# Kernel optimization log

Measured on AMD Instinct MI355X. Metric: run time of the kernel, lower is better.

The kernel has to match this reference:

```python
import jax, jax.numpy as jnp
import numpy as np

EPS = 1e-12  # torch F.normalize default eps


def _l2norm(x):
    n = jnp.sqrt(jnp.sum(x * x, axis=-1, keepdims=True))
    return x / jnp.maximum(n, EPS)


def setup_inputs() -> dict:
    key = jax.random.key(0)
    ks = jax.random.split(key, 8)
    B, T, V = 4, 2048, 512
    C, H, NB = 512, 4, 64
    return {
        "x": jax.random.normal(ks[0], (B, T, V), dtype=jnp.float32),
        "basis": jax.random.normal(ks[1], (V, 2 * NB), dtype=jnp.float32),
        "shared_q_w": jax.random.normal(ks[2], (V, C), dtype=jnp.float32) * 0.02,
        "shared_k_w": jax.random.normal(ks[3], (V, C), dtype=jnp.float32) * 0.02,
        "v_coeffs": jax.random.normal(ks[4], (C, 2 * NB), dtype=jnp.float32) * 0.02,
        "o_coeffs": jax.random.normal(ks[5], (C, 2 * NB), dtype=jnp.float32) * 0.02,
        "decay_logits": jnp.linspace(1.0, 5.0, H, dtype=jnp.float32),
        "out_scale": jnp.float32(0.1),
    }


def reference(x, basis, shared_q_w, shared_k_w, v_coeffs, o_coeffs, decay_logits, out_scale):
    B, T, V = x.shape
    H = decay_logits.shape[0]
    C = shared_q_w.shape[1]
    D = C // H

    v_w = basis @ v_coeffs.T  # [V, C]
    o_w = basis @ o_coeffs.T  # [V, C]

    q = _l2norm(x @ shared_q_w)  # [B, T, C]
    k = _l2norm(x @ shared_k_w)
    v = x @ v_w

    # [B, H, T, D]
    q = q.reshape(B, T, H, D).transpose(0, 2, 1, 3)
    k = k.reshape(B, T, H, D).transpose(0, 2, 1, 3)
    v = v.reshape(B, T, H, D).transpose(0, 2, 1, 3)

    scores = jnp.einsum("bhqd,bhkd->bhqk", q, k)  # [B, H, T, T]

    decay = jax.nn.sigmoid(decay_logits)  # [H]
    pos = jnp.arange(T)
    diff = pos[None, :] - pos[:, None]  # diff[i, j] = j - i
    mask = (diff > 0).astype(scores.dtype)  # [T, T]
    expo = jnp.clip(diff.astype(jnp.float32) - 1.0, 0.0, None)  # [T, T]
    decay_w = (decay[:, None, None] ** expo[None]) * mask[None]  # [H, T, T]

    scores = scores * decay_w[None].astype(scores.dtype)
    retrieved = jnp.einsum("bhqk,bhkd->bhqd", scores, v)  # [B, H, T, D]
    retrieved = retrieved.transpose(0, 2, 1, 3).reshape(B, T, C)
    return retrieved @ o_w.T * out_scale  # [B, T, V]
```

## Files before the change

kernel.cpp:

```cpp
#include <hip/hip_runtime.h>
#include <hip/hip_bf16.h>

#define BB 4
#define TT 2048
#define VV 512
#define CC 512
#define HH 4
#define DD 128
#define NB2 128
#define NROWS (BB*TT)
#define QC 64
#define NCH (TT/QC)
#define SST 66
#define EPS 1e-12f

typedef __attribute__((ext_vector_type(8))) short bf16x8;
typedef __attribute__((ext_vector_type(4))) float f32x4;
typedef unsigned short u16;

__device__ __forceinline__ void gl_lds16(const void* g, void* l) {
    __builtin_amdgcn_global_load_lds(
        (const __attribute__((address_space(1))) unsigned int*)g,
        (__attribute__((address_space(3))) unsigned int*)l, 16, 0, 0);
}
__device__ __forceinline__ u16 f2bu(float x) {
    __hip_bfloat16 h = __float2bfloat16(x);
    return *reinterpret_cast<u16*>(&h);
}
__device__ __forceinline__ float bu2f(u16 u) {
    __hip_bfloat16 h = *reinterpret_cast<__hip_bfloat16*>(&u);
    return __bfloat162float(h);
}

#define PREP_CVT   4096
#define PREP_TR    512
#define PREP_CB    64
#define PREP_Z     16
__global__ __launch_bounds__(256) void prep_all(
    const float* __restrict__ x, const float* __restrict__ qw,
    const float* __restrict__ kw, const float* __restrict__ basis,
    const float* __restrict__ v_coeffs, const float* __restrict__ o_coeffs,
    const float* __restrict__ out_scale,
    u16* __restrict__ xb, u16* __restrict__ wq, u16* __restrict__ wk,
    u16* __restrict__ bab, u16* __restrict__ vcb, u16* __restrict__ ocb,
    float* __restrict__ norms)
{
    __shared__ float tile[32][33];
    const int bi = blockIdx.x, t = threadIdx.x;
    if (bi < PREP_CVT) {
        int i = bi * 256 + t;
        float4 v = ((const float4*)x)[i];
        u16 h[4] = {f2bu(v.x), f2bu(v.y), f2bu(v.z), f2bu(v.w)};
        ((uint2*)xb)[i] = *(uint2*)h;
    } else if (bi < PREP_CVT + PREP_TR) {
        int id = bi - PREP_CVT;
        const int z = id >> 8; id &= 255;
        const float* in = z ? kw : qw;
        u16* outT = z ? wk : wq;
        const int bx = (id & 15) * 32, by = (id >> 4) * 32;
        const int tx = t & 31, ty = t >> 5;
        #pragma unroll
        for (int r = 0; r < 32; r += 8)
            tile[ty + r][tx] = in[(size_t)(by + ty + r) * CC + bx + tx];
        __syncthreads();
        #pragma unroll
        for (int r = 0; r < 32; r += 8)
            outT[(size_t)(bx + ty + r) * VV + by + tx] = f2bu(tile[tx][ty + r]);
    } else if (bi < PREP_CVT + PREP_TR + 3 * PREP_CB) {
        int id = bi - PREP_CVT - PREP_TR;
        const int which = id / PREP_CB;
        int i = (id - which * PREP_CB) * 256 + t;
        const float* src = which == 0 ? basis : (which == 1 ? v_coeffs : o_coeffs);
        u16* dst = which == 0 ? bab : (which == 1 ? vcb : ocb);
        const float sc = which == 2 ? out_scale[0] : 1.f;
        float4 v = ((const float4*)src)[i];
        u16 h[4] = {f2bu(v.x * sc), f2bu(v.y * sc), f2bu(v.z * sc), f2bu(v.w * sc)};
        ((uint2*)dst)[i] = *(uint2*)h;
    } else {
        int idx = (bi - PREP_CVT - PREP_TR - 3 * PREP_CB) * 256 + t;
        ((float4*)norms)[idx] = make_float4(0.f, 0.f, 0.f, 0.f);
    }
}

__device__ __forceinline__ void gemm_body(
    const u16* __restrict__ A, const u16* __restrict__ Bt,
    u16* __restrict__ Cp, int N, int K, int m0, int n0,
    u16* __restrict__ As, u16* __restrict__ Bs)
{
    const int t = threadIdx.x;
    const int wave = t >> 6, lane = t & 63;
    const int qq = lane >> 4, l16 = lane & 15;
    const int wm = (wave >> 1) * 64, wn = (wave & 1) * 64;

    const int s0 = wave * 128 + lane, s1 = s0 + 64;
    const int r0_ = s0 >> 2, c0_ = ((s0 & 3) - (r0_ >> 1)) & 3;
    const int r1_ = s1 >> 2, c1_ = ((s1 & 3) - (r1_ >> 1)) & 3;
    const u16* ga0 = A  + (size_t)(m0 + r0_) * K + c0_ * 8;
    const u16* ga1 = A  + (size_t)(m0 + r1_) * K + c1_ * 8;
    const u16* gb0 = Bt + (size_t)(n0 + r0_) * K + c0_ * 8;
    const u16* gb1 = Bt + (size_t)(n0 + r1_) * K + c1_ * 8;
    const int lo0 = (wave * 128) * 8, lo1 = (wave * 128 + 64) * 8;

    gl_lds16(ga0, As + lo0);
    gl_lds16(ga1, As + lo1);
    gl_lds16(gb0, Bs + lo0);
    gl_lds16(gb1, Bs + lo1);

    f32x4 acc[4][4];
    #pragma unroll
    for (int i = 0; i < 4; ++i)
        #pragma unroll
        for (int j = 0; j < 4; ++j) acc[i][j] = (f32x4){0.f, 0.f, 0.f, 0.f};

    int ib = 0;
    for (int k0 = 0; k0 < K; k0 += 32, ib ^= 1) {
        __syncthreads();
        if (k0 + 32 < K) {
            const int off = (ib ^ 1) * 4096;
            gl_lds16(ga0 + k0 + 32, As + off + lo0);
            gl_lds16(ga1 + k0 + 32, As + off + lo1);
            gl_lds16(gb0 + k0 + 32, Bs + off + lo0);
            gl_lds16(gb1 + k0 + 32, Bs + off + lo1);
        }
        const u16* Ac = As + ib * 4096;
        const u16* Bc = Bs + ib * 4096;
        bf16x8 af[4], bfr[4];
        #pragma unroll
        for (int mt = 0; mt < 4; ++mt) {
            const int r = wm + mt * 16 + l16;
            af[mt] = *(const bf16x8*)&Ac[(r * 4 + ((qq + (r >> 1)) & 3)) * 8];
        }
        #pragma unroll
        for (int nt = 0; nt < 4; ++nt) {
            const int r = wn + nt * 16 + l16;
            bfr[nt] = *(const bf16x8*)&Bc[(r * 4 + ((qq + (r >> 1)) & 3)) * 8];
        }
        #pragma unroll
        for (int mt = 0; mt < 4; ++mt)
            #pragma unroll
            for (int nt = 0; nt < 4; ++nt)
                acc[mt][nt] = __builtin_amdgcn_mfma_f32_16x16x32_bf16(
                    af[mt], bfr[nt], acc[mt][nt], 0, 0, 0);
    }
    #pragma unroll
    for (int mt = 0; mt < 4; ++mt)
        #pragma unroll
        for (int r = 0; r < 4; ++r) {
            int grow = m0 + wm + mt * 16 + qq * 4 + r;
            #pragma unroll
            for (int nt = 0; nt < 4; ++nt)
                Cp[(size_t)grow * N + n0 + wn + nt * 16 + l16] = f2bu(acc[mt][nt][r]);
        }
}

__global__ __launch_bounds__(256) void gemm_w(
    const u16* __restrict__ bab, const u16* __restrict__ vcb,
    const u16* __restrict__ ocb, u16* __restrict__ v_wT, u16* __restrict__ o_ws)
{
    __shared__ __align__(16) u16 As[8192];
    __shared__ __align__(16) u16 Bs[8192];
    const int sec = blockIdx.x >> 2;
    const u16* A  = sec ? bab : vcb;
    const u16* Bt = sec ? ocb : bab;
    u16* C = sec ? o_ws : v_wT;
    gemm_body(A, Bt, C, 512, NB2, blockIdx.y * 128, (blockIdx.x & 3) * 128, As, Bs);
}

__global__ __launch_bounds__(256, 1) void gemm_qkv_fused(
    const u16* __restrict__ xb, const u16* __restrict__ wcat,
    u16* __restrict__ qo, u16* __restrict__ ko, u16* __restrict__ vo,
    float* __restrict__ norms)
{
    __shared__ __align__(16) u16 As[2 * 4096];
    __shared__ __align__(16) u16 Bs[3 * 2 * 4096];
    const int t = threadIdx.x;
    const int wave = t >> 6, lane = t & 63;
    const int qq = lane >> 4, l16 = lane & 15;
    const int m0 = blockIdx.y * 128, n0 = blockIdx.x * 128;
    const int wm = (wave >> 1) * 64, wn = (wave & 1) * 64;
    const int K = VV;

    const int s0 = wave * 128 + lane, s1 = s0 + 64;
    const int r0_ = s0 >> 2, c0_ = ((s0 & 3) - (r0_ >> 1)) & 3;
    const int r1_ = s1 >> 2, c1_ = ((s1 & 3) - (r1_ >> 1)) & 3;
    const u16* ga0 = xb + (size_t)(m0 + r0_) * K + c0_ * 8;
    const u16* ga1 = xb + (size_t)(m0 + r1_) * K + c1_ * 8;
    const u16* gb0[3];
    const u16* gb1[3];
    #pragma unroll
    for (int sec = 0; sec < 3; ++sec) {
        gb0[sec] = wcat + (size_t)sec * VV * CC + (size_t)(n0 + r0_) * K + c0_ * 8;
        gb1[sec] = wcat + (size_t)sec * VV * CC + (size_t)(n0 + r1_) * K + c1_ * 8;
    }
    const int lo0 = (wave * 128) * 8, lo1 = lo0 + 512;

    gl_lds16(ga0, As + lo0);
    gl_lds16(ga1, As + lo1);
    #pragma unroll
    for (int sec = 0; sec < 3; ++sec) {
        gl_lds16(gb0[sec], Bs + sec * 8192 + lo0);
        gl_lds16(gb1[sec], Bs + sec * 8192 + lo1);
    }

    f32x4 acc[3][4][4];
    #pragma unroll
    for (int s = 0; s < 3; ++s)
        #pragma unroll
        for (int i = 0; i < 4; ++i)
            #pragma unroll
            for (int j = 0; j < 4; ++j) acc[s][i][j] = (f32x4){0.f, 0.f, 0.f, 0.f};

    int ib = 0;
    for (int k0 = 0; k0 < K; k0 += 32, ib ^= 1) {
        __syncthreads();
        if (k0 + 32 < K) {
            const int off = (ib ^ 1) * 4096;
            gl_lds16(ga0 + k0 + 32, As + off + lo0);
            gl_lds16(ga1 + k0 + 32, As + off + lo1);
            #pragma unroll
            for (int sec = 0; sec < 3; ++sec) {
                gl_lds16(gb0[sec] + k0 + 32, Bs + sec * 8192 + off + lo0);
                gl_lds16(gb1[sec] + k0 + 32, Bs + sec * 8192 + off + lo1);
            }
        }
        const u16* Ac = As + ib * 4096;
        bf16x8 af[4];
        #pragma unroll
        for (int mt = 0; mt < 4; ++mt) {
            const int r = wm + mt * 16 + l16;
            af[mt] = *(const bf16x8*)&Ac[(r * 4 + ((qq + (r >> 1)) & 3)) * 8];
        }
        #pragma unroll
        for (int sec = 0; sec < 3; ++sec) {
            const u16* Bc = Bs + sec * 8192 + ib * 4096;
            bf16x8 bfr[4];
            #pragma unroll
            for (int nt = 0; nt < 4; ++nt) {
                const int r = wn + nt * 16 + l16;
                bfr[nt] = *(const bf16x8*)&Bc[(r * 4 + ((qq + (r >> 1)) & 3)) * 8];
            }
            #pragma unroll
            for (int mt = 0; mt < 4; ++mt)
                #pragma unroll
                for (int nt = 0; nt < 4; ++nt)
                    acc[sec][mt][nt] = __builtin_amdgcn_mfma_f32_16x16x32_bf16(
                        af[mt], bfr[nt], acc[sec][mt][nt], 0, 0, 0);
        }
    }
    #pragma unroll
    for (int sec = 0; sec < 3; ++sec) {
        u16* outp = sec == 0 ? qo : (sec == 1 ? ko : vo);
        #pragma unroll
        for (int mt = 0; mt < 4; ++mt)
            #pragma unroll
            for (int r = 0; r < 4; ++r) {
                int grow = m0 + wm + mt * 16 + qq * 4 + r;
                #pragma unroll
                for (int nt = 0; nt < 4; ++nt)
                    outp[(size_t)grow * CC + n0 + wn + nt * 16 + l16] =
                        f2bu(acc[sec][mt][nt][r]);
            }
        if (sec < 2) {
            float* np = sec == 0 ? norms : norms + NROWS;
            #pragma unroll
            for (int mt = 0; mt < 4; ++mt)
                #pragma unroll
                for (int r = 0; r < 4; ++r) {
                    float s = 0.f;
                    #pragma unroll
                    for (int nt = 0; nt < 4; ++nt) {
                        float v = acc[sec][mt][nt][r];
                        s = fmaf(v, v, s);
                    }
                    s += __shfl_xor(s, 1, 64);
                    s += __shfl_xor(s, 2, 64);
                    s += __shfl_xor(s, 4, 64);
                    s += __shfl_xor(s, 8, 64);
                    if (l16 == 0)
                        atomicAdd(&np[m0 + wm + mt * 16 + qq * 4 + r], s);
                }
        }
    }
}

__global__ __launch_bounds__(256) void gemm_out64(
    const u16* __restrict__ A, const u16* __restrict__ Bt, float* __restrict__ C)
{
    __shared__ __align__(16) u16 As[4096];
    __shared__ __align__(16) u16 Bs[8192];
    const int t = threadIdx.x;
    const int wave = t >> 6, lane = t & 63;
    const int qq = lane >> 4, l16 = lane & 15;
    const int m0 = blockIdx.y * 64, n0 = blockIdx.x * 128;
    const int wm = (wave >> 1) * 32, wn = (wave & 1) * 64;
    const int N = VV, K = CC;

    const int sA = wave * 64 + lane;
    const int rA = sA >> 2, cA = ((sA & 3) - (rA >> 1)) & 3;
    const int sB0 = wave * 128 + lane, sB1 = sB0 + 64;
    const int rB0 = sB0 >> 2, cB0 = ((sB0 & 3) - (rB0 >> 1)) & 3;
    const int rB1 = sB1 >> 2, cB1 = ((sB1 & 3) - (rB1 >> 1)) & 3;
    const u16* ga  = A  + (size_t)(m0 + rA) * K + cA * 8;
    const u16* gb0 = Bt + (size_t)(n0 + rB0) * K + cB0 * 8;
    const u16* gb1 = Bt + (size_t)(n0 + rB1) * K + cB1 * 8;
    const int loA = wave * 512, loB0 = wave * 1024, loB1 = wave * 1024 + 512;

    gl_lds16(ga, As + loA);
    gl_lds16(gb0, Bs + loB0);
    gl_lds16(gb1, Bs + loB1);

    f32x4 acc[2][4];
    #pragma unroll
    for (int i = 0; i < 2; ++i)
        #pragma unroll
        for (int j = 0; j < 4; ++j) acc[i][j] = (f32x4){0.f, 0.f, 0.f, 0.f};

    int ib = 0;
    for (int k0 = 0; k0 < K; k0 += 32, ib ^= 1) {
        __syncthreads();
        if (k0 + 32 < K) {
            gl_lds16(ga + k0 + 32,  As + (ib ^ 1) * 2048 + loA);
            gl_lds16(gb0 + k0 + 32, Bs + (ib ^ 1) * 4096 + loB0);
            gl_lds16(gb1 + k0 + 32, Bs + (ib ^ 1) * 4096 + loB1);
        }
        const u16* Ac = As + ib * 2048;
        const u16* Bc = Bs + ib * 4096;
        bf16x8 af[2], bfr[4];
        #pragma unroll
        for (int mt = 0; mt < 2; ++mt) {
            const int r = wm + mt * 16 + l16;
            af[mt] = *(const bf16x8*)&Ac[(r * 4 + ((qq + (r >> 1)) & 3)) * 8];
        }
        #pragma unroll
        for (int nt = 0; nt < 4; ++nt) {
            const int r = wn + nt * 16 + l16;
            bfr[nt] = *(const bf16x8*)&Bc[(r * 4 + ((qq + (r >> 1)) & 3)) * 8];
        }
        #pragma unroll
        for (int mt = 0; mt < 2; ++mt)
            #pragma unroll
            for (int nt = 0; nt < 4; ++nt)
                acc[mt][nt] = __builtin_amdgcn_mfma_f32_16x16x32_bf16(
                    af[mt], bfr[nt], acc[mt][nt], 0, 0, 0);
    }
    #pragma unroll
    for (int mt = 0; mt < 2; ++mt)
        #pragma unroll
        for (int r = 0; r < 4; ++r) {
            int grow = m0 + wm + mt * 16 + qq * 4 + r;
            #pragma unroll
            for (int nt = 0; nt < 4; ++nt)
                C[(size_t)grow * N + n0 + wn + nt * 16 + l16] = acc[mt][nt][r];
        }
}

__global__ __launch_bounds__(256) void state_local(
    const u16* __restrict__ kb, const u16* __restrict__ vb,
    const float* __restrict__ norms_k, const float* __restrict__ dlog,
    u16* __restrict__ statesb)
{
    __shared__ __align__(16) u16 vT[DD][SST];
    __shared__ __align__(16) u16 kT[DD][SST];
    const int c = blockIdx.x, bh = blockIdx.y;
    const int b = bh >> 2, h = bh & 3;
    const float lam = 1.f / (1.f + __expf(-dlog[h]));
    const float l2lam = log2f(lam);
    const int t = threadIdx.x;
    const int row0 = b * TT + c * QC;
    const size_t gbase = (size_t)row0 * CC + h * DD;

    {
        const int j2 = t & 31, d0 = (t >> 5) * 16;
        const int jj0 = 2 * j2, jj1 = jj0 + 1;
        const float w0 = exp2f((float)jj0 * l2lam);
        const float w1 = exp2f((float)jj1 * l2lam);
        const float rk0 = 1.f / fmaxf(sqrtf(norms_k[row0 + jj0]), EPS);
        const float rk1 = 1.f / fmaxf(sqrtf(norms_k[row0 + jj1]), EPS);
        u16 k0a[16], k1a[16], v0a[16], v1a[16];
        const u16* k0p = kb + gbase + (size_t)jj0 * CC + d0;
        const u16* k1p = kb + gbase + (size_t)jj1 * CC + d0;
        const u16* v0p = vb + gbase + (size_t)jj0 * CC + d0;
        const u16* v1p = vb + gbase + (size_t)jj1 * CC + d0;
        *(uint4*)&k0a[0] = *(const uint4*)k0p; *(uint4*)&k0a[8] = *(const uint4*)(k0p + 8);
        *(uint4*)&k1a[0] = *(const uint4*)k1p; *(uint4*)&k1a[8] = *(const uint4*)(k1p + 8);
        *(uint4*)&v0a[0] = *(const uint4*)v0p; *(uint4*)&v0a[8] = *(const uint4*)(v0p + 8);
        *(uint4*)&v1a[0] = *(const uint4*)v1p; *(uint4*)&v1a[8] = *(const uint4*)(v1p + 8);
        #pragma unroll
        for (int i = 0; i < 16; ++i) {
            unsigned int kw = (unsigned int)f2bu(bu2f(k0a[i]) * rk0)
                            | ((unsigned int)f2bu(bu2f(k1a[i]) * rk1) << 16);
            *(unsigned int*)&kT[d0 + i][jj0] = kw;
            unsigned int vw = (unsigned int)f2bu(bu2f(v0a[i]) * w0)
                            | ((unsigned int)f2bu(bu2f(v1a[i]) * w1) << 16);
            *(unsigned int*)&vT[d0 + i][jj0] = vw;
        }
    }
    __syncthreads();

    const int wave = t >> 6, lane = t & 63;
    const int quad = lane >> 4, l16 = lane & 15;
    f32x4 acc[2][8];
    #pragma unroll
    for (int i = 0; i < 2; ++i)
        #pragma unroll
        for (int j = 0; j < 8; ++j) acc[i][j] = (f32x4){0.f, 0.f, 0.f, 0.f};

    #pragma unroll
    for (int s = 0; s < 2; ++s) {
        bf16x8 af[2];
        #pragma unroll
        for (int mt = 0; mt < 2; ++mt)
            af[mt] = *(const bf16x8*)&vT[wave * 32 + mt * 16 + l16][s * 32 + quad * 8];
        #pragma unroll
        for (int nt = 0; nt < 8; ++nt) {
            bf16x8 bk = *(const bf16x8*)&kT[nt * 16 + l16][s * 32 + quad * 8];
            #pragma unroll
            for (int mt = 0; mt < 2; ++mt)
                acc[mt][nt] = __builtin_amdgcn_mfma_f32_16x16x32_bf16(
                    af[mt], bk, acc[mt][nt], 0, 0, 0);
        }
    }
    u16* so = statesb + ((size_t)(bh * NCH + c) << 14);
    #pragma unroll
    for (int mt = 0; mt < 2; ++mt)
        #pragma unroll
        for (int rr = 0; rr < 4; ++rr) {
            const int d = wave * 32 + mt * 16 + quad * 4 + rr;
            #pragma unroll
            for (int nt = 0; nt < 8; ++nt)
                so[(size_t)d * DD + nt * 16 + l16] = f2bu(acc[mt][nt][rr]);
        }
}

__global__ __launch_bounds__(256) void state_combine(
    const float* __restrict__ dlog, u16* __restrict__ statesb)
{
    const int bh = blockIdx.x >> 3, part = blockIdx.x & 7;
    const int h = bh & 3;
    const float lam = 1.f / (1.f + __expf(-dlog[h]));
    const float lamQ = exp2f((float)QC * log2f(lam));
    const int t = threadIdx.x;
    float run[8] = {};
    uint4* pbase = (uint4*)(statesb + ((size_t)(bh * NCH) << 14)) + part * 256 + t;
    uint4 cur = pbase[(size_t)(NCH - 1) * 2048];
    for (int c = NCH - 1; c >= 0; --c) {
        uint4 nxt = cur;
        if (c) nxt = pbase[(size_t)(c - 1) * 2048];
        u16* hb = (u16*)&cur;
        uint4 outw;
        u16* ho = (u16*)&outw;
        #pragma unroll
        for (int i = 0; i < 8; ++i) {
            float tmp = bu2f(hb[i]);
            ho[i] = f2bu(run[i]);
            run[i] = fmaf(lamQ, run[i], tmp);
        }
        pbase[(size_t)c * 2048] = outw;
        cur = nxt;
    }
}

__global__ __launch_bounds__(256) void attention_fused(
    const u16* __restrict__ qb, const u16* __restrict__ kb,
    const u16* __restrict__ vb, const u16* __restrict__ statesb,
    const float* __restrict__ norms, const float* __restrict__ dlog,
    u16* __restrict__ retb)
{
    __shared__ __align__(16) u16 qks[2 * QC * DD];
    __shared__ __align__(16) u16 vsT[DD][SST];
    __shared__ __align__(16) u16 ss[QC][SST];
    __shared__ float rql[QC], rkl[QC];

    const int c = blockIdx.x, bh = blockIdx.y;
    const int b = bh >> 2, h = bh & 3;
    const float lam = 1.f / (1.f + __expf(-dlog[h]));
    const float l2lam = log2f(lam);
    const int t = threadIdx.x;
    const int row0 = b * TT + c * QC;
    const size_t base = (size_t)row0 * CC + h * DD;

    const int wave = t >> 6, lane = t & 63;
    const int quad = lane >> 4, l16 = lane & 15;
    const int r0 = wave * 16;

    {
        const int lrow = lane >> 4, cch = lane & 15;
        #pragma unroll
        for (int u = 0; u < 4; ++u) {
            const int R = wave * 16 + u * 4;
            const int gr = R + lrow;
            const int cq = (cch - gr) & 15;
            gl_lds16(qb + base + (size_t)gr * CC + cq * 8, &qks[R * DD]);
            gl_lds16(kb + base + (size_t)gr * CC + cq * 8, &qks[(QC + R) * DD]);
        }
    }
    if (t < QC)            rql[t]      = 1.f / fmaxf(sqrtf(norms[row0 + t]), EPS);
    else if (t < 2 * QC)   rkl[t - QC] = 1.f / fmaxf(sqrtf(norms[NROWS + row0 + t - QC]), EPS);
    {
        const int j2 = t & 31, d0 = (t >> 5) * 16;
        const u16* v0 = vb + base + (size_t)(2 * j2) * CC + d0;
        const u16* v1 = v0 + CC;
        uint4 a0 = *(const uint4*)v0;
        uint4 a1 = *(const uint4*)(v0 + 8);
        uint4 b0 = *(const uint4*)v1;
        uint4 b1 = *(const uint4*)(v1 + 8);
        const u16* ap0 = (const u16*)&a0; const u16* ap1 = (const u16*)&a1;
        const u16* bp0 = (const u16*)&b0; const u16* bp1 = (const u16*)&b1;
        #pragma unroll
        for (int i = 0; i < 8; ++i) {
            *(unsigned int*)&vsT[d0 + i][2 * j2] =
                (unsigned int)ap0[i] | ((unsigned int)bp0[i] << 16);
            *(unsigned int*)&vsT[d0 + 8 + i][2 * j2] =
                (unsigned int)ap1[i] | ((unsigned int)bp1[i] << 16);
        }
    }
    __syncthreads();

    bf16x8 aq[4];
    #pragma unroll
    for (int kq = 0; kq < 4; ++kq) {
        const int r = r0 + l16;
        aq[kq] = *(const bf16x8*)&qks[r * DD + ((kq * 4 + quad + r) & 15) * 8];
    }

    f32x4 accs[4];
    #pragma unroll
    for (int nt = 0; nt < 4; ++nt) accs[nt] = (f32x4){0.f, 0.f, 0.f, 0.f};
    #pragma unroll
    for (int nt = 0; nt < 4; ++nt)
        #pragma unroll
        for (int kq = 0; kq < 4; ++kq) {
            const int rk_ = nt * 16 + l16;
            bf16x8 bk = *(const bf16x8*)&qks[(QC + rk_) * DD + ((kq * 4 + quad + rk_) & 15) * 8];
            accs[nt] = __builtin_amdgcn_mfma_f32_16x16x32_bf16(aq[kq], bk, accs[nt], 0, 0, 0);
        }

    #pragma unroll
    for (int nt = 0; nt < 4; ++nt) {
        const int j = nt * 16 + l16;
        const float rkj = rkl[j];
        #pragma unroll
        for (int rr = 0; rr < 4; ++rr) {
            const int i = r0 + quad * 4 + rr;
            const int di = j - i;
            float p = (di > 0) ? accs[nt][rr] * exp2f((float)(di - 1) * l2lam) * rkj : 0.f;
            ss[i][j] = f2bu(p);
        }
    }
    __syncthreads();

    const u16* sb = statesb + ((size_t)(bh * NCH + c) << 14);
    {
        const int drow = lane >> 4, cch = lane & 15;
        #pragma unroll
        for (int u = 0; u < 8; ++u) {
            const int D = wave * 32 + u * 4;
            const int gd = D + drow;
            const int cq = (cch - gd) & 15;
            gl_lds16(sb + (size_t)gd * DD + cq * 8, &qks[D * DD]);
        }
    }
    bf16x8 ap[2];
    #pragma unroll
    for (int kj = 0; kj < 2; ++kj)
        ap[kj] = *(const bf16x8*)&ss[r0 + l16][kj * 32 + quad * 8];
    f32x4 accd[8];
    #pragma unroll
    for (int nt = 0; nt < 8; ++nt) accd[nt] = (f32x4){0.f, 0.f, 0.f, 0.f};
    #pragma unroll
    for (int nt = 0; nt < 8; ++nt)
        #pragma unroll
        for (int kj = 0; kj < 2; ++kj) {
            bf16x8 bv = *(const bf16x8*)&vsT[nt * 16 + l16][kj * 32 + quad * 8];
            accd[nt] = __builtin_amdgcn_mfma_f32_16x16x32_bf16(ap[kj], bv, accd[nt], 0, 0, 0);
        }
    __syncthreads();

    f32x4 accc[8];
    #pragma unroll
    for (int nt = 0; nt < 8; ++nt) accc[nt] = (f32x4){0.f, 0.f, 0.f, 0.f};
    #pragma unroll
    for (int nt = 0; nt < 8; ++nt)
        #pragma unroll
        for (int kq = 0; kq < 4; ++kq) {
            const int d = nt * 16 + l16;
            bf16x8 bs_ = *(const bf16x8*)&qks[d * DD + ((kq * 4 + quad + d) & 15) * 8];
            accc[nt] = __builtin_amdgcn_mfma_f32_16x16x32_bf16(aq[kq], bs_, accc[nt], 0, 0, 0);
        }

    u16* rb = retb + (size_t)row0 * CC + h * DD;
    #pragma unroll
    for (int rr = 0; rr < 4; ++rr) {
        const int ii = r0 + quad * 4 + rr;
        const float wrow = exp2f((float)(QC - 1 - ii) * l2lam);
        const float rq = rql[ii];
        #pragma unroll
        for (int nt = 0; nt < 8; ++nt) {
            float val = (accd[nt][rr] + wrow * accc[nt][rr]) * rq;
            rb[(size_t)ii * CC + nt * 16 + l16] = f2bu(val);
        }
    }
}

extern "C" void kernel_launch(void* const* d_in, const int* in_sizes, int n_in,
                              void* d_out, int out_size, void* d_ws, size_t ws_size,
                              hipStream_t stream) {
    const float* x         = (const float*)d_in[0];
    const float* basis     = (const float*)d_in[1];
    const float* qw        = (const float*)d_in[2];
    const float* kw        = (const float*)d_in[3];
    const float* v_coeffs  = (const float*)d_in[4];
    const float* o_coeffs  = (const float*)d_in[5];
    const float* dlog      = (const float*)d_in[6];
    const float* out_scale = (const float*)d_in[7];
    float* out             = (float*)d_out;

    u16* p = (u16*)d_ws;
    u16* qb      = p;
    u16* kb      = qb + (size_t)NROWS * CC;
    u16* vb      = kb + (size_t)NROWS * CC;
    u16* statesb = vb + (size_t)NROWS * CC;
    u16* xb      = statesb + (size_t)BB * HH * NCH * DD * DD;
    u16* retb    = xb;
    u16* wcat    = xb + (size_t)NROWS * CC;
    u16* o_ws    = wcat + 3 * (size_t)VV * CC;
    float* norms = (float*)(o_ws + (size_t)VV * CC);
    u16* bab     = (u16*)(norms + 2 * NROWS);
    u16* vcb     = bab + (size_t)VV * NB2;
    u16* ocb     = vcb + (size_t)VV * NB2;

    prep_all<<<PREP_CVT + PREP_TR + 3 * PREP_CB + PREP_Z, 256, 0, stream>>>(
        x, qw, kw, basis, v_coeffs, o_coeffs, out_scale,
        xb, wcat, wcat + (size_t)VV * CC, bab, vcb, ocb, norms);
    gemm_w<<<dim3(8, 4), 256, 0, stream>>>(bab, vcb, ocb,
                                           wcat + 2 * (size_t)VV * CC, o_ws);
    gemm_qkv_fused<<<dim3(4, NROWS / 128), 256, 0, stream>>>(xb, wcat, qb, kb, vb,
                                                             norms);
    state_local  <<<dim3(NCH, BB * HH), 256, 0, stream>>>(kb, vb, norms + NROWS,
                                                          dlog, statesb);
    state_combine<<<BB * HH * 8, 256, 0, stream>>>(dlog, statesb);
    attention_fused<<<dim3(NCH, BB * HH), 256, 0, stream>>>(qb, kb, vb, statesb,
                                                            norms, dlog, retb);
    gemm_out64<<<dim3(VV / 128, NROWS / 64), 256, 0, stream>>>(retb, o_ws, out);
}
```

Baseline: 168.0 us.

## Fuse weight GEMM into prep kernel and merge tail stages into one cooperative kernel

```diff
diff --git a/kernel.cpp b/kernel.cpp
--- a/kernel.cpp
+++ b/kernel.cpp
@@ -1,5 +1,8 @@
 #include <hip/hip_runtime.h>
 #include <hip/hip_bf16.h>
+#include <hip/hip_cooperative_groups.h>
+
+namespace cg = cooperative_groups;
 
 #define BB 4
 #define TT 2048
@@ -31,29 +34,36 @@
     __hip_bfloat16 h = *reinterpret_cast<__hip_bfloat16*>(&u);
     return __bfloat162float(h);
 }
-
-#define PREP_CVT   4096
-#define PREP_TR    512
-#define PREP_CB    64
-#define PREP_Z     16
-__global__ __launch_bounds__(256) void prep_all(
+__device__ __forceinline__ uint4 pack8(float4 a, float4 b, float s) {
+    u16 h[8] = {f2bu(a.x * s), f2bu(a.y * s), f2bu(a.z * s), f2bu(a.w * s),
+                f2bu(b.x * s), f2bu(b.y * s), f2bu(b.z * s), f2bu(b.w * s)};
+    return *(uint4*)h;
+}
+
+#define P2_CVT 4096
+#define P2_TR  512
+#define P2_Z   16
+#define P2_WG  32
+__global__ __launch_bounds__(256) void prep_all2(
     const float* __restrict__ x, const float* __restrict__ qw,
     const float* __restrict__ kw, const float* __restrict__ basis,
     const float* __restrict__ v_coeffs, const float* __restrict__ o_coeffs,
     const float* __restrict__ out_scale,
     u16* __restrict__ xb, u16* __restrict__ wq, u16* __restrict__ wk,
-    u16* __restrict__ bab, u16* __restrict__ vcb, u16* __restrict__ ocb,
-    float* __restrict__ norms)
+    u16* __restrict__ v_wT, u16* __restrict__ o_ws, float* __restrict__ norms)
 {
-    __shared__ float tile[32][33];
+    __shared__ __align__(16) union {
+        float tile[32][33];
+        struct { u16 A[4096]; u16 B[4096]; } w;
+    } sm;
     const int bi = blockIdx.x, t = threadIdx.x;
-    if (bi < PREP_CVT) {
+    if (bi < P2_CVT) {
         int i = bi * 256 + t;
         float4 v = ((const float4*)x)[i];
         u16 h[4] = {f2bu(v.x), f2bu(v.y), f2bu(v.z), f2bu(v.w)};
         ((uint2*)xb)[i] = *(uint2*)h;
-    } else if (bi < PREP_CVT + PREP_TR) {
-        int id = bi - PREP_CVT;
+    } else if (bi < P2_CVT + P2_TR) {
+        int id = bi - P2_CVT;
         const int z = id >> 8; id &= 255;
         const float* in = z ? kw : qw;
         u16* outT = z ? wk : wq;
@@ -61,109 +71,74 @@
         const int tx = t & 31, ty = t >> 5;
         #pragma unroll
         for (int r = 0; r < 32; r += 8)
-            tile[ty + r][tx] = in[(size_t)(by + ty + r) * CC + bx + tx];
+            sm.tile[ty + r][tx] = in[(size_t)(by + ty + r) * CC + bx + tx];
         __syncthreads();
         #pragma unroll
         for (int r = 0; r < 32; r += 8)
-            outT[(size_t)(bx + ty + r) * VV + by + tx] = f2bu(tile[tx][ty + r]);
-    } else if (bi < PREP_CVT + PREP_TR + 3 * PREP_CB) {
-        int id = bi - PREP_CVT - PREP_TR;
-        const int which = id / PREP_CB;
-        int i = (id - which * PREP_CB) * 256 + t;
-        const float* src = which == 0 ? basis : (which == 1 ? v_coeffs : o_coeffs);
-        u16* dst = which == 0 ? bab : (which == 1 ? vcb : ocb);
-        const float sc = which == 2 ? out_scale[0] : 1.f;
-        float4 v = ((const float4*)src)[i];
-        u16 h[4] = {f2bu(v.x * sc), f2bu(v.y * sc), f2bu(v.z * sc), f2bu(v.w * sc)};
-        ((uint2*)dst)[i] = *(uint2*)h;
+            outT[(size_t)(bx + ty + r) * VV + by + tx] = f2bu(sm.tile[tx][ty + r]);
+    } else if (bi < P2_CVT + P2_TR + P2_Z) {
+        int idx = (bi - P2_CVT - P2_TR) * 256 + t;
+        ((float4*)norms)[idx] = make_float4(0.f, 0.f, 0.f, 0.f);
     } else {
-        int idx = (bi - PREP_CVT - PREP_TR - 3 * PREP_CB) * 256 + t;
-        ((float4*)norms)[idx] = make_float4(0.f, 0.f, 0.f, 0.f);
-    }
-}
-
-__device__ __forceinline__ void gemm_body(
-    const u16* __restrict__ A, const u16* __restrict__ Bt,
-    u16* __restrict__ Cp, int N, int K, int m0, int n0,
-    u16* __restrict__ As, u16* __restrict__ Bs)
-{
-    const int t = threadIdx.x;
-    const int wave = t >> 6, lane = t & 63;
-    const int qq = lane >> 4, l16 = lane & 15;
-    const int wm = (wave >> 1) * 64, wn = (wave & 1) * 64;
-
-    const int s0 = wave * 128 + lane, s1 = s0 + 64;
-    const int r0_ = s0 >> 2, c0_ = ((s0 & 3) - (r0_ >> 1)) & 3;
-    const int r1_ = s1 >> 2, c1_ = ((s1 & 3) - (r1_ >> 1)) & 3;
-    const u16* ga0 = A  + (size_t)(m0 + r0_) * K + c0_ * 8;
-    const u16* ga1 = A  + (size_t)(m0 + r1_) * K + c1_ * 8;
-    const u16* gb0 = Bt + (size_t)(n0 + r0_) * K + c0_ * 8;
-    const u16* gb1 = Bt + (size_t)(n0 + r1_) * K + c1_ * 8;
-    const int lo0 = (wave * 128) * 8, lo1 = (wave * 128 + 64) * 8;
-
-    gl_lds16(ga0, As + lo0);
-    gl_lds16(ga1, As + lo1);
-    gl_lds16(gb0, Bs + lo0);
-    gl_lds16(gb1, Bs + lo1);
-
-    f32x4 acc[4][4];
-    #pragma unroll
-    for (int i = 0; i < 4; ++i)
-        #pragma unroll
-        for (int j = 0; j < 4; ++j) acc[i][j] = (f32x4){0.f, 0.f, 0.f, 0.f};
-
-    int ib = 0;
-    for (int k0 = 0; k0 < K; k0 += 32, ib ^= 1) {
-        __syncthreads();
-        if (k0 + 32 < K) {
-            const int off = (ib ^ 1) * 4096;
-            gl_lds16(ga0 + k0 + 32, As + off + lo0);
-            gl_lds16(ga1 + k0 + 32, As + off + lo1);
-            gl_lds16(gb0 + k0 + 32, Bs + off + lo0);
-            gl_lds16(gb1 + k0 + 32, Bs + off + lo1);
-        }
-        const u16* Ac = As + ib * 4096;
-        const u16* Bc = Bs + ib * 4096;
-        bf16x8 af[4], bfr[4];
-        #pragma unroll
-        for (int mt = 0; mt < 4; ++mt) {
-            const int r = wm + mt * 16 + l16;
-            af[mt] = *(const bf16x8*)&Ac[(r * 4 + ((qq + (r >> 1)) & 3)) * 8];
-        }
-        #pragma unroll
-        for (int nt = 0; nt < 4; ++nt) {
-            const int r = wn + nt * 16 + l16;
-            bfr[nt] = *(const bf16x8*)&Bc[(r * 4 + ((qq + (r >> 1)) & 3)) * 8];
+        int id = bi - (P2_CVT + P2_TR + P2_Z);
+        const int sec = id >> 4, rem = id & 15;
+        const int m0 = (rem >> 2) * 128, n0 = (rem & 3) * 128;
+        const float* Af = sec ? basis : v_coeffs;
+        const float* Bf = sec ? o_coeffs : basis;
+        u16* Cp = sec ? o_ws : v_wT;
+        const float scB = sec ? out_scale[0] : 1.f;
+        const int wave = t >> 6, lane = t & 63;
+        const int qq = lane >> 4, l16 = lane & 15;
+        const int wm = (wave >> 1) * 64, wn = (wave & 1) * 64;
+        const int s0 = wave * 128 + lane, s1 = s0 + 64;
+        const int r0 = s0 >> 2, c0 = ((s0 & 3) - (r0 >> 1)) & 3;
+        const int r1 = s1 >> 2, c1 = ((s1 & 3) - (r1 >> 1)) & 3;
+        f32x4 acc[4][4];
+        #pragma unroll
+        for (int i = 0; i < 4; ++i)
+            #pragma unroll
+            for (int j = 0; j < 4; ++j) acc[i][j] = (f32x4){0.f, 0.f, 0.f, 0.f};
+        for (int k0 = 0; k0 < NB2; k0 += 32) {
+            __syncthreads();
+            {
+                const float* p0 = Af + (size_t)(m0 + r0) * NB2 + k0 + c0 * 8;
+                const float* p1 = Af + (size_t)(m0 + r1) * NB2 + k0 + c1 * 8;
+                *(uint4*)&sm.w.A[s0 * 8] = pack8(((const float4*)p0)[0], ((const float4*)p0)[1], 1.f);
+                *(uint4*)&sm.w.A[s1 * 8] = pack8(((const float4*)p1)[0], ((const float4*)p1)[1], 1.f);
+                const float* q0 = Bf + (size_t)(n0 + r0) * NB2 + k0 + c0 * 8;
+                const float* q1 = Bf + (size_t)(n0 + r1) * NB2 + k0 + c1 * 8;
+                *(uint4*)&sm.w.B[s0 * 8] = pack8(((const float4*)q0)[0], ((const float4*)q0)[1], scB);
+                *(uint4*)&sm.w.B[s1 * 8] = pack8(((const float4*)q1)[0], ((const float4*)q1)[1], scB);
+            }
+            __syncthreads();
+            bf16x8 af[4], bfr[4];
+            #pragma unroll
+            for (int mt = 0; mt < 4; ++mt) {
+                const int r = wm + mt * 16 + l16;
+                af[mt] = *(const bf16x8*)&sm.w.A[(r * 4 + ((qq + (r >> 1)) & 3)) * 8];
+            }
+            #pragma unroll
+            for (int nt = 0; nt < 4; ++nt) {
+                const int r = wn + nt * 16 + l16;
+                bfr[nt] = *(const bf16x8*)&sm.w.B[(r * 4 + ((qq + (r >> 1)) & 3)) * 8];
+            }
+            #pragma unroll
+            for (int mt = 0; mt < 4; ++mt)
+                #pragma unroll
+                for (int nt = 0; nt < 4; ++nt)
+                    acc[mt][nt] = __builtin_amdgcn_mfma_f32_16x16x32_bf16(
+                        af[mt], bfr[nt], acc[mt][nt], 0, 0, 0);
         }
         #pragma unroll
         for (int mt = 0; mt < 4; ++mt)
             #pragma unroll
-            for (int nt = 0; nt < 4; ++nt)
-                acc[mt][nt] = __builtin_amdgcn_mfma_f32_16x16x32_bf16(
-                    af[mt], bfr[nt], acc[mt][nt], 0, 0, 0);
-    }
-    #pragma unroll
-    for (int mt = 0; mt < 4; ++mt)
-        #pragma unroll
-        for (int r = 0; r < 4; ++r) {
-            int grow = m0 + wm + mt * 16 + qq * 4 + r;
-            #pragma unroll
-            for (int nt = 0; nt < 4; ++nt)
-                Cp[(size_t)grow * N + n0 + wn + nt * 16 + l16] = f2bu(acc[mt][nt][r]);
-        }
-}
-
-__global__ __launch_bounds__(256) void gemm_w(
-    const u16* __restrict__ bab, const u16* __restrict__ vcb,
-    const u16* __restrict__ ocb, u16* __restrict__ v_wT, u16* __restrict__ o_ws)
-{
-    __shared__ __align__(16) u16 As[8192];
-    __shared__ __align__(16) u16 Bs[8192];
-    const int sec = blockIdx.x >> 2;
-    const u16* A  = sec ? bab : vcb;
-    const u16* Bt = sec ? ocb : bab;
-    u16* C = sec ? o_ws : v_wT;
-    gemm_body(A, Bt, C, 512, NB2, blockIdx.y * 128, (blockIdx.x & 3) * 128, As, Bs);
+            for (int rr = 0; rr < 4; ++rr) {
+                int grow = m0 + wm + mt * 16 + qq * 4 + rr;
+                #pragma unroll
+                for (int nt = 0; nt < 4; ++nt)
+                    Cp[(size_t)grow * 512 + n0 + wn + nt * 16 + l16] = f2bu(acc[mt][nt][rr]);
+            }
+    }
 }
 
 __global__ __launch_bounds__(256, 1) void gemm_qkv_fused(
@@ -283,322 +258,305 @@
     }
 }
 
-__global__ __launch_bounds__(256) void gemm_out64(
-    const u16* __restrict__ A, const u16* __restrict__ Bt, float* __restrict__ C)
+__global__ __launch_bounds__(256, 2) void tail_coop(
+    const u16* __restrict__ qb, const u16* __restrict__ kb,
+    const u16* __restrict__ vb, u16* __restrict__ statesb,
+    const float* __restrict__ norms, const float* __restrict__ dlog,
+    u16* __restrict__ retb, const u16* __restrict__ o_ws,
+    float* __restrict__ out)
 {
-    __shared__ __align__(16) u16 As[4096];
-    __shared__ __align__(16) u16 Bs[8192];
+    cg::grid_group gg = cg::this_grid();
+    __shared__ __align__(16) union {
+        struct { u16 vT[DD][SST]; u16 kT[DD][SST]; } pa;
+        struct { u16 qks[2 * QC * DD]; u16 vsT[DD][SST]; u16 ss[QC][SST];
+                 float rql[QC]; float rkl[QC]; } pc;
+        struct { u16 As[4096]; u16 Bs[8192]; } pd;
+    } sm;
+
     const int t = threadIdx.x;
     const int wave = t >> 6, lane = t & 63;
-    const int qq = lane >> 4, l16 = lane & 15;
-    const int m0 = blockIdx.y * 64, n0 = blockIdx.x * 128;
-    const int wm = (wave >> 1) * 32, wn = (wave & 1) * 64;
-    const int N = VV, K = CC;
-
-    const int sA = wave * 64 + lane;
-    const int rA = sA >> 2, cA = ((sA & 3) - (rA >> 1)) & 3;
-    const int sB0 = wave * 128 + lane, sB1 = sB0 + 64;
-    const int rB0 = sB0 >> 2, cB0 = ((sB0 & 3) - (rB0 >> 1)) & 3;
-    const int rB1 = sB1 >> 2, cB1 = ((sB1 & 3) - (rB1 >> 1)) & 3;
-    const u16* ga  = A  + (size_t)(m0 + rA) * K + cA * 8;
-    const u16* gb0 = Bt + (size_t)(n0 + rB0) * K + cB0 * 8;
-    const u16* gb1 = Bt + (size_t)(n0 + rB1) * K + cB1 * 8;
-    const int loA = wave * 512, loB0 = wave * 1024, loB1 = wave * 1024 + 512;
-
-    gl_lds16(ga, As + loA);
-    gl_lds16(gb0, Bs + loB0);
-    gl_lds16(gb1, Bs + loB1);
-
-    f32x4 acc[2][4];
-    #pragma unroll
-    for (int i = 0; i < 2; ++i)
-        #pragma unroll
-        for (int j = 0; j < 4; ++j) acc[i][j] = (f32x4){0.f, 0.f, 0.f, 0.f};
-
-    int ib = 0;
-    for (int k0 = 0; k0 < K; k0 += 32, ib ^= 1) {
-        __syncthreads();
-        if (k0 + 32 < K) {
-            gl_lds16(ga + k0 + 32,  As + (ib ^ 1) * 2048 + loA);
-            gl_lds16(gb0 + k0 + 32, Bs + (ib ^ 1) * 4096 + loB0);
-            gl_lds16(gb1 + k0 + 32, Bs + (ib ^ 1) * 4096 + loB1);
-        }
-        const u16* Ac = As + ib * 2048;
-        const u16* Bc = Bs + ib * 4096;
-        bf16x8 af[2], bfr[4];
-        #pragma unroll
-        for (int mt = 0; mt < 2; ++mt) {
-            const int r = wm + mt * 16 + l16;
-            af[mt] = *(const bf16x8*)&Ac[(r * 4 + ((qq + (r >> 1)) & 3)) * 8];
-        }
-        #pragma unroll
-        for (int nt = 0; nt < 4; ++nt) {
-            const int r = wn + nt * 16 + l16;
-            bfr[nt] = *(const bf16x8*)&Bc[(r * 4 + ((qq + (r >> 1)) & 3)) * 8];
-        }
-        #pragma unroll
-        for (int mt = 0; mt < 2; ++mt)
-            #pragma unroll
-            for (int nt = 0; nt < 4; ++nt)
-                acc[mt][nt] = __builtin_amdgcn_mfma_f32_16x16x32_bf16(
-                    af[mt], bfr[nt], acc[mt][nt], 0, 0, 0);
-    }
-    #pragma unroll
-    for (int mt = 0; mt < 2; ++mt)
-        #pragma unroll
-        for (int r = 0; r < 4; ++r) {
-            int grow = m0 + wm + mt * 16 + qq * 4 + r;
-            #pragma unroll
-            for (int nt = 0; nt < 4; ++nt)
-                C[(size_t)grow * N + n0 + wn + nt * 16 + l16] = acc[mt][nt][r];
-        }
-}
-
-__global__ __launch_bounds__(256) void state_local(
-    const u16* __restrict__ kb, const u16* __restrict__ vb,
-    const float* __restrict__ norms_k, const float* __restrict__ dlog,
-    u16* __restrict__ statesb)
-{
-    __shared__ __align__(16) u16 vT[DD][SST];
-    __shared__ __align__(16) u16 kT[DD][SST];
-    const int c = blockIdx.x, bh = blockIdx.y;
+    const int quad = lane >> 4, l16 = lane & 15;
+    const int cx = blockIdx.x, bh = blockIdx.y;
     const int b = bh >> 2, h = bh & 3;
     const float lam = 1.f / (1.f + __expf(-dlog[h]));
     const float l2lam = log2f(lam);
-    const int t = threadIdx.x;
-    const int row0 = b * TT + c * QC;
-    const size_t gbase = (size_t)row0 * CC + h * DD;
 
     {
-        const int j2 = t & 31, d0 = (t >> 5) * 16;
-        const int jj0 = 2 * j2, jj1 = jj0 + 1;
-        const float w0 = exp2f((float)jj0 * l2lam);
-        const float w1 = exp2f((float)jj1 * l2lam);
-        const float rk0 = 1.f / fmaxf(sqrtf(norms_k[row0 + jj0]), EPS);
-        const float rk1 = 1.f / fmaxf(sqrtf(norms_k[row0 + jj1]), EPS);
-        u16 k0a[16], k1a[16], v0a[16], v1a[16];
-        const u16* k0p = kb + gbase + (size_t)jj0 * CC + d0;
-        const u16* k1p = kb + gbase + (size_t)jj1 * CC + d0;
-        const u16* v0p = vb + gbase + (size_t)jj0 * CC + d0;
-        const u16* v1p = vb + gbase + (size_t)jj1 * CC + d0;
-        *(uint4*)&k0a[0] = *(const uint4*)k0p; *(uint4*)&k0a[8] = *(const uint4*)(k0p + 8);
-        *(uint4*)&k1a[0] = *(const uint4*)k1p; *(uint4*)&k1a[8] = *(const uint4*)(k1p + 8);
-        *(uint4*)&v0a[0] = *(const uint4*)v0p; *(uint4*)&v0a[8] = *(const uint4*)(v0p + 8);
-        *(uint4*)&v1a[0] = *(const uint4*)v1p; *(uint4*)&v1a[8] = *(const uint4*)(v1p + 8);
-        #pragma unroll
-        for (int i = 0; i < 16; ++i) {
-            unsigned int kw = (unsigned int)f2bu(bu2f(k0a[i]) * rk0)
-                            | ((unsigned int)f2bu(bu2f(k1a[i]) * rk1) << 16);
-            *(unsigned int*)&kT[d0 + i][jj0] = kw;
-            unsigned int vw = (unsigned int)f2bu(bu2f(v0a[i]) * w0)
-                            | ((unsigned int)f2bu(bu2f(v1a[i]) * w1) << 16);
-            *(unsigned int*)&vT[d0 + i][jj0] = vw;
-        }
-    }
-    __syncthreads();
-
-    const int wave = t >> 6, lane = t & 63;
-    const int quad = lane >> 4, l16 = lane & 15;
-    f32x4 acc[2][8];
-    #pragma unroll
-    for (int i = 0; i < 2; ++i)
-        #pragma unroll
-        for (int j = 0; j < 8; ++j) acc[i][j] = (f32x4){0.f, 0.f, 0.f, 0.f};
-
-    #pragma unroll
-    for (int s = 0; s < 2; ++s) {
-        bf16x8 af[2];
+        const int row0 = b * TT + cx * QC;
+        const size_t gbase = (size_t)row0 * CC + h * DD;
+        {
+            const int j2 = t & 31, d0 = (t >> 5) * 16;
+            const int jj0 = 2 * j2, jj1 = jj0 + 1;
+            const float w0 = exp2f((float)jj0 * l2lam);
+            const float w1 = exp2f((float)jj1 * l2lam);
+            const float rk0 = 1.f / fmaxf(sqrtf(norms[NROWS + row0 + jj0]), EPS);
+            const float rk1 = 1.f / fmaxf(sqrtf(norms[NROWS + row0 + jj1]), EPS);
+            u16 k0a[16], k1a[16], v0a[16], v1a[16];
+            const u16* k0p = kb + gbase + (size_t)jj0 * CC + d0;
+            const u16* k1p = kb + gbase + (size_t)jj1 * CC + d0;
+            const u16* v0p = vb + gbase + (size_t)jj0 * CC + d0;
+            const u16* v1p = vb + gbase + (size_t)jj1 * CC + d0;
+            *(uint4*)&k0a[0] = *(const uint4*)k0p; *(uint4*)&k0a[8] = *(const uint4*)(k0p + 8);
+            *(uint4*)&k1a[0] = *(const uint4*)k1p; *(uint4*)&k1a[8] = *(const uint4*)(k1p + 8);
+            *(uint4*)&v0a[0] = *(const uint4*)v0p; *(uint4*)&v0a[8] = *(const uint4*)(v0p + 8);
+            *(uint4*)&v1a[0] = *(const uint4*)v1p; *(uint4*)&v1a[8] = *(const uint4*)(v1p + 8);
+            #pragma unroll
+            for (int i = 0; i < 16; ++i) {
+                unsigned int kw = (unsigned int)f2bu(bu2f(k0a[i]) * rk0)
+                                | ((unsigned int)f2bu(bu2f(k1a[i]) * rk1) << 16);
+                *(unsigned int*)&sm.pa.kT[d0 + i][jj0] = kw;
+                unsigned int vw = (unsigned int)f2bu(bu2f(v0a[i]) * w0)
+                                | ((unsigned int)f2bu(bu2f(v1a[i]) * w1) << 16);
+                *(unsigned int*)&sm.pa.vT[d0 + i][jj0] = vw;
+            }
+        }
+        __syncthreads();
+
+        f32x4 acc[2][8];
+        #pragma unroll
+        for (int i = 0; i < 2; ++i)
+            #pragma unroll
+            for (int j = 0; j < 8; ++j) acc[i][j] = (f32x4){0.f, 0.f, 0.f, 0.f};
+
+        #pragma unroll
+        for (int s = 0; s < 2; ++s) {
+            bf16x8 af[2];
+            #pragma unroll
+            for (int mt = 0; mt < 2; ++mt)
+                af[mt] = *(const bf16x8*)&sm.pa.vT[wave * 32 + mt * 16 + l16][s * 32 + quad * 8];
+            #pragma unroll
+            for (int nt = 0; nt < 8; ++nt) {
+                bf16x8 bk = *(const bf16x8*)&sm.pa.kT[nt * 16 + l16][s * 32 + quad * 8];
+                #pragma unroll
+                for (int mt = 0; mt < 2; ++mt)
+                    acc[mt][nt] = __builtin_amdgcn_mfma_f32_16x16x32_bf16(
+                        af[mt], bk, acc[mt][nt], 0, 0, 0);
+            }
+        }
+        u16* so = statesb + ((size_t)(bh * NCH + cx) << 14);
         #pragma unroll
         for (int mt = 0; mt < 2; ++mt)
-            af[mt] = *(const bf16x8*)&vT[wave * 32 + mt * 16 + l16][s * 32 + quad * 8];
-        #pragma unroll
-        for (int nt = 0; nt < 8; ++nt) {
-            bf16x8 bk = *(const bf16x8*)&kT[nt * 16 + l16][s * 32 + quad * 8];
+            #pragma unroll
+            for (int rr = 0; rr < 4; ++rr) {
+                const int d = wave * 32 + mt * 16 + quad * 4 + rr;
+                #pragma unroll
+                for (int nt = 0; nt < 8; ++nt)
+                    so[(size_t)d * DD + nt * 16 + l16] = f2bu(acc[mt][nt][rr]);
+            }
+    }
+    __threadfence();
+    gg.sync();
+
+    {
+        const float lamQ = exp2f((float)QC * l2lam);
+        unsigned int* pb = (unsigned int*)(statesb + ((size_t)(bh * NCH) << 14))
+                           + cx * 256 + t;
+        float run0 = 0.f, run1 = 0.f;
+        unsigned int cur = pb[(size_t)(NCH - 1) * 8192];
+        for (int c2 = NCH - 1; c2 >= 0; --c2) {
+            unsigned int nxt = cur;
+            if (c2) nxt = pb[(size_t)(c2 - 1) * 8192];
+            float t0 = bu2f((u16)(cur & 0xffffu));
+            float t1 = bu2f((u16)(cur >> 16));
+            unsigned int outw = (unsigned int)f2bu(run0)
+                              | ((unsigned int)f2bu(run1) << 16);
+            pb[(size_t)c2 * 8192] = outw;
+            run0 = fmaf(lamQ, run0, t0);
+            run1 = fmaf(lamQ, run1, t1);
+            cur = nxt;
+        }
+    }
+    __threadfence();
+    gg.sync();
+
+    {
+        const int row0 = b * TT + cx * QC;
+        const size_t base = (size_t)row0 * CC + h * DD;
+        const int r0 = wave * 16;
+        {
+            const int lrow = lane >> 4, cch = lane & 15;
+            #pragma unroll
+            for (int u = 0; u < 4; ++u) {
+                const int R = wave * 16 + u * 4;
+                const int gr = R + lrow;
+                const int cq = (cch - gr) & 15;
+                gl_lds16(qb + base + (size_t)gr * CC + cq * 8, &sm.pc.qks[R * DD]);
+                gl_lds16(kb + base + (size_t)gr * CC + cq * 8, &sm.pc.qks[(QC + R) * DD]);
+            }
+        }
+        if (t < QC)            sm.pc.rql[t]      = 1.f / fmaxf(sqrtf(norms[row0 + t]), EPS);
+        else if (t < 2 * QC)   sm.pc.rkl[t - QC] = 1.f / fmaxf(sqrtf(norms[NROWS + row0 + t - QC]), EPS);
+        {
+            const int j2 = t & 31, d0 = (t >> 5) * 16;
+            const u16* v0 = vb + base + (size_t)(2 * j2) * CC + d0;
+            const u16* v1 = v0 + CC;
+            uint4 a0 = *(const uint4*)v0;
+            uint4 a1 = *(const uint4*)(v0 + 8);
+            uint4 b0 = *(const uint4*)v1;
+            uint4 b1 = *(const uint4*)(v1 + 8);
+            const u16* ap0 = (const u16*)&a0; const u16* ap1 = (const u16*)&a1;
+            const u16* bp0 = (const u16*)&b0; const u16* bp1 = (const u16*)&b1;
+            #pragma unroll
+            for (int i = 0; i < 8; ++i) {
+                *(unsigned int*)&sm.pc.vsT[d0 + i][2 * j2] =
+                    (unsigned int)ap0[i] | ((unsigned int)bp0[i] << 16);
+                *(unsigned int*)&sm.pc.vsT[d0 + 8 + i][2 * j2] =
+                    (unsigned int)ap1[i] | ((unsigned int)bp1[i] << 16);
+            }
+        }
+        __syncthreads();
+
+        bf16x8 aq[4];
+        #pragma unroll
+        for (int kq = 0; kq < 4; ++kq) {
+            const int r = r0 + l16;
+            aq[kq] = *(const bf16x8*)&sm.pc.qks[r * DD + ((kq * 4 + quad + r) & 15) * 8];
+        }
+
+        f32x4 accs[4];
+        #pragma unroll
+        for (int nt = 0; nt < 4; ++nt) accs[nt] = (f32x4){0.f, 0.f, 0.f, 0.f};
+        #pragma unroll
+        for (int nt = 0; nt < 4; ++nt)
+            #pragma unroll
+            for (int kq = 0; kq < 4; ++kq) {
+                const int rk_ = nt * 16 + l16;
+                bf16x8 bk = *(const bf16x8*)&sm.pc.qks[(QC + rk_) * DD + ((kq * 4 + quad + rk_) & 15) * 8];
+                accs[nt] = __builtin_amdgcn_mfma_f32_16x16x32_bf16(aq[kq], bk, accs[nt], 0, 0, 0);
+            }
+
+        #pragma unroll
+        for (int nt = 0; nt < 4; ++nt) {
+            const int j = nt * 16 + l16;
+            const float rkj = sm.pc.rkl[j];
+            #pragma unroll
+            for (int rr = 0; rr < 4; ++rr) {
+                const int i = r0 + quad * 4 + rr;
+                const int di = j - i;
+                float p = (di > 0) ? accs[nt][rr] * exp2f((float)(di - 1) * l2lam) * rkj : 0.f;
+                sm.pc.ss[i][j] = f2bu(p);
+            }
+        }
+        __syncthreads();
+
+        const u16* sb = statesb + ((size_t)(bh * NCH + cx) << 14);
+        {
+            const int drow = lane >> 4, cch = lane & 15;
+            #pragma unroll
+            for (int u = 0; u < 8; ++u) {
+                const int D_ = wave * 32 + u * 4;
+                const int gd = D_ + drow;
+                const int cq = (cch - gd) & 15;
+                gl_lds16(sb + (size_t)gd * DD + cq * 8, &sm.pc.qks[D_ * DD]);
+            }
+        }
+        bf16x8 app[2];
+        #pragma unroll
+        for (int kj = 0; kj < 2; ++kj)
+            app[kj] = *(const bf16x8*)&sm.pc.ss[r0 + l16][kj * 32 + quad * 8];
+        f32x4 accd[8];
+        #pragma unroll
+        for (int nt = 0; nt < 8; ++nt) accd[nt] = (f32x4){0.f, 0.f, 0.f, 0.f};
+        #pragma unroll
+        for (int nt = 0; nt < 8; ++nt)
+            #pragma unroll
+            for (int kj = 0; kj < 2; ++kj) {
+                bf16x8 bv = *(const bf16x8*)&sm.pc.vsT[nt * 16 + l16][kj * 32 + quad * 8];
+                accd[nt] = __builtin_amdgcn_mfma_f32_16x16x32_bf16(app[kj], bv, accd[nt], 0, 0, 0);
+            }
+        __syncthreads();
+
+        f32x4 accc[8];
+        #pragma unroll
+        for (int nt = 0; nt < 8; ++nt) accc[nt] = (f32x4){0.f, 0.f, 0.f, 0.f};
+        #pragma unroll
+        for (int nt = 0; nt < 8; ++nt)
+            #pragma unroll
+            for (int kq = 0; kq < 4; ++kq) {
+                const int d = nt * 16 + l16;
+                bf16x8 bs_ = *(const bf16x8*)&sm.pc.qks[d * DD + ((kq * 4 + quad + d) & 15) * 8];
+                accc[nt] = __builtin_amdgcn_mfma_f32_16x16x32_bf16(aq[kq], bs_, accc[nt], 0, 0, 0);
+            }
+
+        u16* rb = retb + (size_t)row0 * CC + h * DD;
+        #pragma unroll
+        for (int rr = 0; rr < 4; ++rr) {
+            const int ii = r0 + quad * 4 + rr;
+            const float wrow = exp2f((float)(QC - 1 - ii) * l2lam);
+            const float rq = sm.pc.rql[ii];
+            #pragma unroll
+            for (int nt = 0; nt < 8; ++nt) {
+                float val = (accd[nt][rr] + wrow * accc[nt][rr]) * rq;
+                rb[(size_t)ii * CC + nt * 16 + l16] = f2bu(val);
+            }
+        }
+    }
+    __threadfence();
+    gg.sync();
+
+    {
+        const int flat = bh * 32 + cx;
+        const int m0 = (flat >> 2) * 64, n0 = (flat & 3) * 128;
+        const int wm = (wave >> 1) * 32, wn = (wave & 1) * 64;
+        const int N = VV, K = CC;
+
+        const int sA = wave * 64 + lane;
+        const int rA = sA >> 2, cA = ((sA & 3) - (rA >> 1)) & 3;
+        const int sB0 = wave * 128 + lane, sB1 = sB0 + 64;
+        const int rB0 = sB0 >> 2, cB0 = ((sB0 & 3) - (rB0 >> 1)) & 3;
+        const int rB1 = sB1 >> 2, cB1 = ((sB1 & 3) - (rB1 >> 1)) & 3;
+        const u16* ga  = retb + (size_t)(m0 + rA) * K + cA * 8;
+        const u16* gb0 = o_ws + (size_t)(n0 + rB0) * K + cB0 * 8;
+        const u16* gb1 = o_ws + (size_t)(n0 + rB1) * K + cB1 * 8;
+        const int loA = wave * 512, loB0 = wave * 1024, loB1 = wave * 1024 + 512;
+
+        gl_lds16(ga, sm.pd.As + loA);
+        gl_lds16(gb0, sm.pd.Bs + loB0);
+        gl_lds16(gb1, sm.pd.Bs + loB1);
+
+        f32x4 acc[2][4];
+        #pragma unroll
+        for (int i = 0; i < 2; ++i)
+            #pragma unroll
+            for (int j = 0; j < 4; ++j) acc[i][j] = (f32x4){0.f, 0.f, 0.f, 0.f};
+
+        int ib = 0;
+        for (int k0 = 0; k0 < K; k0 += 32, ib ^= 1) {
+            __syncthreads();
+            if (k0 + 32 < K) {
+                gl_lds16(ga + k0 + 32,  sm.pd.As + (ib ^ 1) * 2048 + loA);
+                gl_lds16(gb0 + k0 + 32, sm.pd.Bs + (ib ^ 1) * 4096 + loB0);
+                gl_lds16(gb1 + k0 + 32, sm.pd.Bs + (ib ^ 1) * 4096 + loB1);
+            }
+            const u16* Ac = sm.pd.As + ib * 2048;
+            const u16* Bc = sm.pd.Bs + ib * 4096;
+            bf16x8 af[2], bfr[4];
+            #pragma unroll
+            for (int mt = 0; mt < 2; ++mt) {
+                const int r = wm + mt * 16 + l16;
+                af[mt] = *(const bf16x8*)&Ac[(r * 4 + ((quad + (r >> 1)) & 3)) * 8];
+            }
+            #pragma unroll
+            for (int nt = 0; nt < 4; ++nt) {
+                const int r = wn + nt * 16 + l16;
+                bfr[nt] = *(const bf16x8*)&Bc[(r * 4 + ((quad + (r >> 1)) & 3)) * 8];
+            }
             #pragma unroll
             for (int mt = 0; mt < 2; ++mt)
-                acc[mt][nt] = __builtin_amdgcn_mfma_f32_16x16x32_bf16(
-                    af[mt], bk, acc[mt][nt], 0, 0, 0);
-        }
-    }
-    u16* so = statesb + ((size_t)(bh * NCH + c) << 14);
-    #pragma unroll
-    for (int mt = 0; mt < 2; ++mt)
-        #pragma unroll
-        for (int rr = 0; rr < 4; ++rr) {
-            const int d = wave * 32 + mt * 16 + quad * 4 + rr;
-            #pragma unroll
-            for (int nt = 0; nt < 8; ++nt)
-                so[(size_t)d * DD + nt * 16 + l16] = f2bu(acc[mt][nt][rr]);
-        }
-}
-
-__global__ __launch_bounds__(256) void state_combine(
-    const float* __restrict__ dlog, u16* __restrict__ statesb)
-{
-    const int bh = blockIdx.x >> 3, part = blockIdx.x & 7;
-    const int h = bh & 3;
-    const float lam = 1.f / (1.f + __expf(-dlog[h]));
-    const float lamQ = exp2f((float)QC * log2f(lam));
-    const int t = threadIdx.x;
-    float run[8] = {};
-    uint4* pbase = (uint4*)(statesb + ((size_t)(bh * NCH) << 14)) + part * 256 + t;
-    uint4 cur = pbase[(size_t)(NCH - 1) * 2048];
-    for (int c = NCH - 1; c >= 0; --c) {
-        uint4 nxt = cur;
-        if (c) nxt = pbase[(size_t)(c - 1) * 2048];
-        u16* hb = (u16*)&cur;
-        uint4 outw;
-        u16* ho = (u16*)&outw;
-        #pragma unroll
-        for (int i = 0; i < 8; ++i) {
-            float tmp = bu2f(hb[i]);
-            ho[i] = f2bu(run[i]);
-            run[i] = fmaf(lamQ, run[i], tmp);
-        }
-        pbase[(size_t)c * 2048] = outw;
-        cur = nxt;
-    }
-}
-
-__global__ __launch_bounds__(256) void attention_fused(
-    const u16* __restrict__ qb, const u16* __restrict__ kb,
-    const u16* __restrict__ vb, const u16* __restrict__ statesb,
-    const float* __restrict__ norms, const float* __restrict__ dlog,
-    u16* __restrict__ retb)
-{
-    __shared__ __align__(16) u16 qks[2 * QC * DD];
-    __shared__ __align__(16) u16 vsT[DD][SST];
-    __shared__ __align__(16) u16 ss[QC][SST];
-    __shared__ float rql[QC], rkl[QC];
-
-    const int c = blockIdx.x, bh = blockIdx.y;
-    const int b = bh >> 2, h = bh & 3;
-    const float lam = 1.f / (1.f + __expf(-dlog[h]));
-    const float l2lam = log2f(lam);
-    const int t = threadIdx.x;
-    const int row0 = b * TT + c * QC;
-    const size_t base = (size_t)row0 * CC + h * DD;
-
-    const int wave = t >> 6, lane = t & 63;
-    const int quad = lane >> 4, l16 = lane & 15;
-    const int r0 = wave * 16;
-
-    {
-        const int lrow = lane >> 4, cch = lane & 15;
-        #pragma unroll
-        for (int u = 0; u < 4; ++u) {
-            const int R = wave * 16 + u * 4;
-            const int gr = R + lrow;
-            const int cq = (cch - gr) & 15;
-            gl_lds16(qb + base + (size_t)gr * CC + cq * 8, &qks[R * DD]);
-            gl_lds16(kb + base + (size_t)gr * CC + cq * 8, &qks[(QC + R) * DD]);
-        }
-    }
-    if (t < QC)            rql[t]      = 1.f / fmaxf(sqrtf(norms[row0 + t]), EPS);
-    else if (t < 2 * QC)   rkl[t - QC] = 1.f / fmaxf(sqrtf(norms[NROWS + row0 + t - QC]), EPS);
-    {
-        const int j2 = t & 31, d0 = (t >> 5) * 16;
-        const u16* v0 = vb + base + (size_t)(2 * j2) * CC + d0;
-        const u16* v1 = v0 + CC;
-        uint4 a0 = *(const uint4*)v0;
-        uint4 a1 = *(const uint4*)(v0 + 8);
-        uint4 b0 = *(const uint4*)v1;
-        uint4 b1 = *(const uint4*)(v1 + 8);
-        const u16* ap0 = (const u16*)&a0; const u16* ap1 = (const u16*)&a1;
-        const u16* bp0 = (const u16*)&b0; const u16* bp1 = (const u16*)&b1;
-        #pragma unroll
-        for (int i = 0; i < 8; ++i) {
-            *(unsigned int*)&vsT[d0 + i][2 * j2] =
-                (unsigned int)ap0[i] | ((unsigned int)bp0[i] << 16);
-            *(unsigned int*)&vsT[d0 + 8 + i][2 * j2] =
-                (unsigned int)ap1[i] | ((unsigned int)bp1[i] << 16);
-        }
-    }
-    __syncthreads();
-
-    bf16x8 aq[4];
-    #pragma unroll
-    for (int kq = 0; kq < 4; ++kq) {
-        const int r = r0 + l16;
-        aq[kq] = *(const bf16x8*)&qks[r * DD + ((kq * 4 + quad + r) & 15) * 8];
-    }
-
-    f32x4 accs[4];
-    #pragma unroll
-    for (int nt = 0; nt < 4; ++nt) accs[nt] = (f32x4){0.f, 0.f, 0.f, 0.f};
-    #pragma unroll
-    for (int nt = 0; nt < 4; ++nt)
-        #pragma unroll
-        for (int kq = 0; kq < 4; ++kq) {
-            const int rk_ = nt * 16 + l16;
-            bf16x8 bk = *(const bf16x8*)&qks[(QC + rk_) * DD + ((kq * 4 + quad + rk_) & 15) * 8];
-            accs[nt] = __builtin_amdgcn_mfma_f32_16x16x32_bf16(aq[kq], bk, accs[nt], 0, 0, 0);
-        }
-
-    #pragma unroll
-    for (int nt = 0; nt < 4; ++nt) {
-        const int j = nt * 16 + l16;
-        const float rkj = rkl[j];
-        #pragma unroll
-        for (int rr = 0; rr < 4; ++rr) {
-            const int i = r0 + quad * 4 + rr;
-            const int di = j - i;
-            float p = (di > 0) ? accs[nt][rr] * exp2f((float)(di - 1) * l2lam) * rkj : 0.f;
-            ss[i][j] = f2bu(p);
-        }
-    }
-    __syncthreads();
-
-    const u16* sb = statesb + ((size_t)(bh * NCH + c) << 14);
-    {
-        const int drow = lane >> 4, cch = lane & 15;
-        #pragma unroll
-        for (int u = 0; u < 8; ++u) {
-            const int D = wave * 32 + u * 4;
-            const int gd = D + drow;
-            const int cq = (cch - gd) & 15;
-            gl_lds16(sb + (size_t)gd * DD + cq * 8, &qks[D * DD]);
-        }
-    }
-    bf16x8 ap[2];
-    #pragma unroll
-    for (int kj = 0; kj < 2; ++kj)
-        ap[kj] = *(const bf16x8*)&ss[r0 + l16][kj * 32 + quad * 8];
-    f32x4 accd[8];
-    #pragma unroll
-    for (int nt = 0; nt < 8; ++nt) accd[nt] = (f32x4){0.f, 0.f, 0.f, 0.f};
-    #pragma unroll
-    for (int nt = 0; nt < 8; ++nt)
-        #pragma unroll
-        for (int kj = 0; kj < 2; ++kj) {
-            bf16x8 bv = *(const bf16x8*)&vsT[nt * 16 + l16][kj * 32 + quad * 8];
-            accd[nt] = __builtin_amdgcn_mfma_f32_16x16x32_bf16(ap[kj], bv, accd[nt], 0, 0, 0);
-        }
-    __syncthreads();
-
-    f32x4 accc[8];
-    #pragma unroll
-    for (int nt = 0; nt < 8; ++nt) accc[nt] = (f32x4){0.f, 0.f, 0.f, 0.f};
-    #pragma unroll
-    for (int nt = 0; nt < 8; ++nt)
-        #pragma unroll
-        for (int kq = 0; kq < 4; ++kq) {
-            const int d = nt * 16 + l16;
-            bf16x8 bs_ = *(const bf16x8*)&qks[d * DD + ((kq * 4 + quad + d) & 15) * 8];
-            accc[nt] = __builtin_amdgcn_mfma_f32_16x16x32_bf16(aq[kq], bs_, accc[nt], 0, 0, 0);
-        }
-
-    u16* rb = retb + (size_t)row0 * CC + h * DD;
-    #pragma unroll
-    for (int rr = 0; rr < 4; ++rr) {
-        const int ii = r0 + quad * 4 + rr;
-        const float wrow = exp2f((float)(QC - 1 - ii) * l2lam);
-        const float rq = rql[ii];
-        #pragma unroll
-        for (int nt = 0; nt < 8; ++nt) {
-            float val = (accd[nt][rr] + wrow * accc[nt][rr]) * rq;
-            rb[(size_t)ii * CC + nt * 16 + l16] = f2bu(val);
-        }
+                #pragma unroll
+                for (int nt = 0; nt < 4; ++nt)
+                    acc[mt][nt] = __builtin_amdgcn_mfma_f32_16x16x32_bf16(
+                        af[mt], bfr[nt], acc[mt][nt], 0, 0, 0);
+        }
+        #pragma unroll
+        for (int mt = 0; mt < 2; ++mt)
+            #pragma unroll
+            for (int r = 0; r < 4; ++r) {
+                int grow = m0 + wm + mt * 16 + quad * 4 + r;
+                #pragma unroll
+                for (int nt = 0; nt < 4; ++nt)
+                    out[(size_t)grow * N + n0 + wn + nt * 16 + l16] = acc[mt][nt][r];
+            }
     }
 }
 
@@ -625,21 +583,17 @@
     u16* wcat    = xb + (size_t)NROWS * CC;
     u16* o_ws    = wcat + 3 * (size_t)VV * CC;
     float* norms = (float*)(o_ws + (size_t)VV * CC);
-    u16* bab     = (u16*)(norms + 2 * NROWS);
-    u16* vcb     = bab + (size_t)VV * NB2;
-    u16* ocb     = vcb + (size_t)VV * NB2;
-
-    prep_all<<<PREP_CVT + PREP_TR + 3 * PREP_CB + PREP_Z, 256, 0, stream>>>(
+
+    prep_all2<<<P2_CVT + P2_TR + P2_Z + P2_WG, 256, 0, stream>>>(
         x, qw, kw, basis, v_coeffs, o_coeffs, out_scale,
-        xb, wcat, wcat + (size_t)VV * CC, bab, vcb, ocb, norms);
-    gemm_w<<<dim3(8, 4), 256, 0, stream>>>(bab, vcb, ocb,
-                                           wcat + 2 * (size_t)VV * CC, o_ws);
+        xb, wcat, wcat + (size_t)VV * CC, wcat + 2 * (size_t)VV * CC, o_ws, norms);
     gemm_qkv_fused<<<dim3(4, NROWS / 128), 256, 0, stream>>>(xb, wcat, qb, kb, vb,
                                                              norms);
-    state_local  <<<dim3(NCH, BB * HH), 256, 0, stream>>>(kb, vb, norms + NROWS,
-                                                          dlog, statesb);
-    state_combine<<<BB * HH * 8, 256, 0, stream>>>(dlog, statesb);
-    attention_fused<<<dim3(NCH, BB * HH), 256, 0, stream>>>(qb, kb, vb, statesb,
-                                                            norms, dlog, retb);
-    gemm_out64<<<dim3(VV / 128, NROWS / 64), 256, 0, stream>>>(retb, o_ws, out);
-}
+    {
+        void* kargs[] = {(void*)&qb, (void*)&kb, (void*)&vb, (void*)&statesb,
+                         (void*)&norms, (void*)&dlog, (void*)&retb, (void*)&o_ws,
+                         (void*)&out};
+        hipLaunchCooperativeKernel(tail_coop, dim3(NCH, BB * HH), dim3(256, 1, 1),
+                                   kargs, 0, stream);
+    }
+}
```

After: 517.5 us. 3.08x slower.
